# Kernel optimization log

Hardware: AMD Instinct MI355X
Metric: run time of the kernel (lower is better)

Reference implementation:

```python
import jax, jax.numpy as jnp
import numpy as np

H = 16  # num_heads

def setup_inputs() -> dict:
    key = jax.random.key(0)
    ks = jax.random.split(key, 5)
    B, L, D = 2, 2048, 1024
    x = jax.random.normal(ks[0], (B, L, D), dtype=jnp.float32)
    # causal mask: masked_fill where mask == 0
    attn_mask = jnp.tril(jnp.ones((L, L), dtype=jnp.int32))
    scale = 1.0 / np.sqrt(D)
    Wq = jax.random.normal(ks[1], (D, D), dtype=jnp.float32) * scale
    Wk = jax.random.normal(ks[2], (D, D), dtype=jnp.float32) * scale
    Wv = jax.random.normal(ks[3], (D, D), dtype=jnp.float32) * scale
    Wo = jax.random.normal(ks[4], (D, D), dtype=jnp.float32) * scale
    return {"x": x, "attn_mask": attn_mask, "Wq": Wq, "Wk": Wk, "Wv": Wv, "Wo": Wo}

def reference(x, attn_mask, Wq, Wk, Wv, Wo):
    B, L, D = x.shape
    dh = D // H
    # nn.Linear with no bias: y = x @ W^T
    q = (x @ Wq.T).reshape(B, L, H, dh)
    k = (x @ Wk.T).reshape(B, L, H, dh)
    v = (x @ Wv.T).reshape(B, L, H, dh)
    # scores: [B, H, L, L]
    scores = jnp.einsum('blhd,bmhd->bhlm', q, k) / jnp.sqrt(jnp.array(dh, x.dtype))
    scores = jnp.where(attn_mask == 0, -jnp.inf, scores)
    attn = jax.nn.softmax(scores, axis=-1)
    out = jnp.einsum('bhlm,bmhd->blhd', attn, v).reshape(B, L, D)
    return out @ Wo.T
```

## Files before the change

### kernel.cpp

```cpp
#include <hip/hip_runtime.h>
#include <math.h>

#define L_SEQ  2048
#define D_MODEL 1024
#define N_HEAD 16
#define D_HEAD 64
#define B_SIZE 2

typedef __attribute__((ext_vector_type(8))) short bf16x8;
typedef __attribute__((ext_vector_type(4))) float f32x4;
typedef unsigned short u16;
typedef unsigned int u32;

__device__ __forceinline__ f32x4 mfma16(bf16x8 a, bf16x8 b, f32x4 c) {
    return __builtin_amdgcn_mfma_f32_16x16x32_bf16(a, b, c, 0, 0, 0);
}

__device__ __forceinline__ u16 f2bf(float x) {
    u32 u = __builtin_bit_cast(u32, x);
    u32 r = (u + 0x7FFFu + ((u >> 16) & 1u)) >> 16;
    return (u16)r;
}
__device__ __forceinline__ u16 f2bf_t(float x) {
    return (u16)(__builtin_bit_cast(u32, x) >> 16);
}
__device__ __forceinline__ float bf2f(u16 h) {
    u32 u = ((u32)h) << 16;
    return __builtin_bit_cast(float, u);
}

__device__ __forceinline__ void gl2lds16(const void* g, void* l) {
    __builtin_amdgcn_global_load_lds(
        (__attribute__((address_space(1))) void*)(g),
        (__attribute__((address_space(3))) void*)(l), 16, 0, 0);
}

__global__ __launch_bounds__(256) void split_all(
    const float* __restrict__ x,
    const float* __restrict__ w0, const float* __restrict__ w1,
    const float* __restrict__ w2, const float* __restrict__ w3,
    u16* __restrict__ x2, u16* __restrict__ wout) {
    const int id = blockIdx.x;
    const float* in;
    u16* out;
    int idx;
    if (id < 4096) {
        in = x; out = x2; idx = id * 256 + threadIdx.x;
    } else {
        const int wi = (id - 4096) >> 10;
        const int blk = (id - 4096) & 1023;
        in = (wi == 0) ? w0 : (wi == 1) ? w1 : (wi == 2) ? w2 : w3;
        out = wout + (size_t)wi * 2097152;
        idx = blk * 256 + threadIdx.x;
    }
    const int c4 = idx << 2;
    const int r = c4 >> 10, c = c4 & 1023;
    float4 v = *(const float4*)(in + c4);
    u16 h0 = f2bf(v.x), h1 = f2bf(v.y), h2 = f2bf(v.z), h3 = f2bf(v.w);
    ushort4 hi = make_ushort4(h0, h1, h2, h3);
    ushort4 lo = make_ushort4(f2bf(v.x - bf2f(h0)), f2bf(v.y - bf2f(h1)),
                              f2bf(v.z - bf2f(h2)), f2bf(v.w - bf2f(h3)));
    *(ushort4*)(out + (size_t)r * 2048 + c) = hi;
    *(ushort4*)(out + (size_t)r * 2048 + 1024 + c) = lo;
}

__device__ __forceinline__ int kaOf(int x) {
    return (((x >> 4) == 1) ? 1024 : 0) + ((x << 6) & 1023);
}
__device__ __forceinline__ int kwOf(int x) {
    return (((x >> 4) == 0) ? 1024 : 0) + ((x << 6) & 1023);
}

#define SBAR()  do { __builtin_amdgcn_sched_barrier(0); \
                     __builtin_amdgcn_s_barrier(); \
                     __builtin_amdgcn_sched_barrier(0); } while (0)

__global__ __launch_bounds__(512) void gemm256_qkv(
    const u16* __restrict__ A2, const u16* __restrict__ Wall,
    u16* __restrict__ Qh, u16* __restrict__ Ql,
    u16* __restrict__ Kh, u16* __restrict__ Kl,
    u16* __restrict__ Vh) {
    extern __shared__ __align__(16) u16 smem[];

    const int t = threadIdx.x, l = t & 63, wid = t >> 6;
    const int id = blockIdx.x;
    const int wg = (id & 7) * 24 + (id >> 3);
    const int mt = wg / 12, ntile = wg % 12;
    const int m0 = mt << 8, n0 = ntile << 8;

    const int wrH = wid >> 2;
    const int wc = (wid & 3) << 6;
    const int bHalf = (wid & 3) >> 1;
    const int brB = (wid & 1) << 6;

    f32x4 acc[8][4];
#pragma unroll
    for (int i = 0; i < 8; ++i)
#pragma unroll
        for (int j = 0; j < 4; ++j) acc[i][j] = (f32x4){0.f, 0.f, 0.f, 0.f};

    const int sr = t >> 3, sc = t & 7;

    auto stageA = [&](int x, int half) {
        const int koff = kaOf(x);
        u16* dst = smem + ((x & 1) * 32768) + half * 8192;
        const u16* srcb = A2 + (size_t)(m0 + half * 128) * 2048 + koff;
#pragma unroll
        for (int p = 0; p < 2; ++p) {
            const int r = sr + p * 64;
            const int ck = sc ^ (r & 7);
            gl2lds16(srcb + (size_t)r * 2048 + ck * 8, dst + (t + p * 512) * 8);
        }
    };
    auto stageB = [&](int x, int half) {
        const int koff = kwOf(x);
        u16* dst = smem + 16384 + ((x & 1) * 32768) + half * 8192;
        const u16* srcb = Wall + (size_t)(n0 + half * 128) * 2048 + koff;
#pragma unroll
        for (int p = 0; p < 2; ++p) {
            const int r = sr + p * 64;
            const int ck = sc ^ (r & 7);
            gl2lds16(srcb + (size_t)r * 2048 + ck * 8, dst + (t + p * 512) * 8);
        }
    };
    auto dsA = [&](int s, int mh, int kc, bf16x8 af[4]) {
        const u16* Ab = smem + s * 32768 + wrH * 8192;
#pragma unroll
        for (int f = 0; f < 4; ++f) {
            const int r = mh * 64 + f * 16 + (l & 15);
            const int c8 = kc * 4 + (l >> 4);
            af[f] = *(const bf16x8*)&Ab[r * 64 + ((c8 ^ (r & 7)) << 3)];
        }
    };
    auto dsB = [&](int s, int kc, bf16x8 bfr[4]) {
        const u16* Bb = smem + 16384 + s * 32768 + bHalf * 8192;
#pragma unroll
        for (int f = 0; f < 4; ++f) {
            const int r = brB + f * 16 + (l & 15);
            const int c8 = kc * 4 + (l >> 4);
            bfr[f] = *(const bf16x8*)&Bb[r * 64 + ((c8 ^ (r & 7)) << 3)];
        }
    };

    stageB(0, 0); stageB(0, 1); stageA(0, 0); stageA(0, 1);
    stageB(1, 0); stageB(1, 1);
    __builtin_amdgcn_sched_barrier(0);
    asm volatile("s_waitcnt vmcnt(4)" ::: "memory");
    __builtin_amdgcn_s_barrier();
    __builtin_amdgcn_sched_barrier(0);

    const int NT = 48;
    bf16x8 breg0[4], breg1[4], af[4];
    for (int tt = 0; tt < NT; ++tt) {
        const int s = tt & 1;
        dsA(s, 0, 0, af); dsB(s, 0, breg0);
        if (tt + 1 < NT) stageA(tt + 1, 0);
        SBAR();
        __builtin_amdgcn_s_setprio(1);
#pragma unroll
        for (int f = 0; f < 4; ++f)
#pragma unroll
            for (int fn = 0; fn < 4; ++fn)
                acc[f][fn] = mfma16(af[f], breg0[fn], acc[f][fn]);
        __builtin_amdgcn_s_setprio(0);
        SBAR();
        dsA(s, 0, 1, af); dsB(s, 1, breg1);
        if (tt + 1 < NT) stageA(tt + 1, 1);
        SBAR();
        __builtin_amdgcn_s_setprio(1);
#pragma unroll
        for (int f = 0; f < 4; ++f)
#pragma unroll
            for (int fn = 0; fn < 4; ++fn)
                acc[f][fn] = mfma16(af[f], breg1[fn], acc[f][fn]);
        __builtin_amdgcn_s_setprio(0);
        SBAR();
        dsA(s, 1, 0, af);
        if (tt + 2 < NT) stageB(tt + 2, 0);
        SBAR();
        __builtin_amdgcn_s_setprio(1);
#pragma unroll
        for (int f = 0; f < 4; ++f)
#pragma unroll
            for (int fn = 0; fn < 4; ++fn)
                acc[4 + f][fn] = mfma16(af[f], breg0[fn], acc[4 + f][fn]);
        __builtin_amdgcn_s_setprio(0);
        SBAR();
        dsA(s, 1, 1, af);
        if (tt + 2 < NT) stageB(tt + 2, 1);
        SBAR();
        __builtin_amdgcn_s_setprio(1);
#pragma unroll
        for (int f = 0; f < 4; ++f)
#pragma unroll
            for (int fn = 0; fn < 4; ++fn)
                acc[4 + f][fn] = mfma16(af[f], breg1[fn], acc[4 + f][fn]);
        __builtin_amdgcn_s_setprio(0);
        __builtin_amdgcn_sched_barrier(0);
        if (tt + 2 < NT) {
            asm volatile("s_waitcnt vmcnt(4)" ::: "memory");
        } else if (tt + 1 < NT) {
            asm volatile("s_waitcnt vmcnt(0)" ::: "memory");
        }
        __builtin_amdgcn_s_barrier();
        __builtin_amdgcn_sched_barrier(0);
    }

#pragma unroll
    for (int fm = 0; fm < 8; ++fm)
#pragma unroll
        for (int fn = 0; fn < 4; ++fn)
#pragma unroll
            for (int rg = 0; rg < 4; ++rg) {
                const int gm = m0 + wrH * 128 + fm * 16 + ((l >> 4) << 2) + rg;
                const int gn = n0 + wc + fn * 16 + (l & 15);
                const int z = gn >> 10, col = gn & 1023;
                float v = acc[fm][fn][rg];
                if (z == 0) v *= 0.125f;
                const int b = gm >> 11, lq = gm & 2047;
                const int h = col >> 6, d = col & 63;
                const size_t oi = (((size_t)(b * 16 + h)) * 2048 + lq) * 64 + d;
                const u16 hi = f2bf(v);
                if (z == 0) { Qh[oi] = hi; Ql[oi] = f2bf(v - bf2f(hi)); }
                else if (z == 1) { Kh[oi] = hi; Kl[oi] = f2bf(v - bf2f(hi)); }
                else { Vh[oi] = hi; }
            }
}

__global__ __launch_bounds__(256) void gemm_wo(
    const u16* __restrict__ A2, const u16* __restrict__ W2,
    float* __restrict__ Cout) {
    __shared__ __align__(16) u16 As[128 * 32];
    __shared__ __align__(16) u16 Ws2[64 * 32];
    const int t = threadIdx.x, l = t & 63, wid = t >> 6;
    const int id = blockIdx.x;
    const int nid = ((id & 7) << 6) + (id >> 3);
    const int m0 = (nid >> 4) << 7;
    const int n0 = (nid & 15) << 6;
    const int wm = wid >> 1, wn = wid & 1;

    f32x4 acc[4][2];
#pragma unroll
    for (int i = 0; i < 4; ++i)
#pragma unroll
        for (int j = 0; j < 2; ++j) acc[i][j] = (f32x4){0.f, 0.f, 0.f, 0.f};

    const int arow0 = t >> 2, ach0 = (t & 3) ^ (arow0 & 3);
    const int arow1 = (t + 256) >> 2, ach1 = (t & 3) ^ (arow1 & 3);
    const int brow = t >> 2, bch = (t & 3) ^ (brow & 3);

    for (int k0 = 0; k0 < 3072; k0 += 32) {
        const int rg3 = k0 >> 10, kb = k0 & 1023;
        const int ka = (rg3 == 1 ? 1024 : 0) + kb;
        const int kw = (rg3 == 0 ? 1024 : 0) + kb;
        __syncthreads();
        gl2lds16(A2 + (size_t)(m0 + arow0) * 2048 + ka + ach0 * 8,
                 (u16*)As + t * 8);
        gl2lds16(A2 + (size_t)(m0 + arow1) * 2048 + ka + ach1 * 8,
                 (u16*)As + (t + 256) * 8);
        if (t < 256)
            gl2lds16(W2 + (size_t)(n0 + brow) * 2048 + kw + bch * 8,
                     (u16*)Ws2 + t * 8);
        __syncthreads();
        bf16x8 af[4], bfr[2];
#pragma unroll
        for (int f = 0; f < 4; ++f) {
            const int row = wm * 64 + f * 16 + (l & 15);
            const int ch = (l >> 4) ^ (row & 3);
            af[f] = *(const bf16x8*)&As[(row << 5) + (ch << 3)];
        }
#pragma unroll
        for (int f = 0; f < 2; ++f) {
            const int rown = wn * 32 + f * 16 + (l & 15);
            const int chn = (l >> 4) ^ (rown & 3);
            bfr[f] = *(const bf16x8*)&Ws2[(rown << 5) + (chn << 3)];
        }
        __builtin_amdgcn_s_setprio(1);
#pragma unroll
        for (int fm = 0; fm < 4; ++fm)
#pragma unroll
            for (int fn = 0; fn < 2; ++fn)
                acc[fm][fn] = mfma16(af[fm], bfr[fn], acc[fm][fn]);
        __builtin_amdgcn_s_setprio(0);
    }

#pragma unroll
    for (int fm = 0; fm < 4; ++fm)
#pragma unroll
        for (int fn = 0; fn < 2; ++fn)
#pragma unroll
            for (int rg = 0; rg < 4; ++rg) {
                const int gm = m0 + wm * 64 + fm * 16 + ((l >> 4) << 2) + rg;
                const int gn = n0 + wn * 32 + fn * 16 + (l & 15);
                Cout[(size_t)gm * 1024 + gn] = acc[fm][fn][rg];
            }
}

__global__ __launch_bounds__(128) void vtrans(const u16* __restrict__ Vh,
                                              u16* __restrict__ Vth) {
    const int t = threadIdx.x;
    const int kt = (blockIdx.x << 1) + (t >> 6);
    const int h = blockIdx.y, b = blockIdx.z;
    const size_t base = ((size_t)(b * 16 + h)) * 131072;
    const int kv0 = kt << 6;
    const int st = t & 63;
    const int r0 = (st >> 3) << 3;
    const int c0 = (st & 7) << 3;
    ushort4 inv[8][2];
#pragma unroll
    for (int j = 0; j < 8; ++j) {
        const u16* p = Vh + base + (size_t)(kv0 + r0 + j) * 64 + c0;
        inv[j][0] = *(const ushort4*)p;
        inv[j][1] = *(const ushort4*)(p + 4);
    }
#pragma unroll
    for (int i = 0; i < 8; ++i) {
        u16 o[8];
#pragma unroll
        for (int j = 0; j < 8; ++j) {
            ushort4 vv = inv[j][i >> 2];
            const int ii = i & 3;
            o[j] = (ii == 0) ? vv.x : (ii == 1) ? vv.y : (ii == 2) ? vv.z : vv.w;
        }
        u16* q = Vth + base + (size_t)(c0 + i) * 2048 + kv0 + r0;
        *(ushort4*)q = make_ushort4(o[0], o[1], o[2], o[3]);
        *(ushort4*)(q + 4) = make_ushort4(o[4], o[5], o[6], o[7]);
    }
}

struct QTileState {
    bf16x8 qhf[2], qlf[2];
    f32x4 oacc[4];
    float mrow[4], lrow[4];
};

__device__ __forceinline__ void qstate_init(
    QTileState& st, const u16* Qh, const u16* Ql, size_t hb, int q0, int w, int l) {
    const int rowq = q0 + (w << 4) + (l & 15);
#pragma unroll
    for (int kc = 0; kc < 2; ++kc) {
        const size_t off = hb + (size_t)rowq * 64 + (((kc << 2) + (l >> 4)) << 3);
        st.qhf[kc] = *(const bf16x8*)(Qh + off);
        st.qlf[kc] = *(const bf16x8*)(Ql + off);
    }
#pragma unroll
    for (int i = 0; i < 4; ++i) {
        st.oacc[i] = (f32x4){0.f, 0.f, 0.f, 0.f};
        st.mrow[i] = -INFINITY;
        st.lrow[i] = 0.f;
    }
}

__device__ __forceinline__ void fa_qk_softmax(
    QTileState& st, const u16* bKh, const u16* bKl,
    int kv0, int q0, int w, int l, u16 pb[4][4]) {
    f32x4 sacc[4];
#pragma unroll
    for (int nf = 0; nf < 4; ++nf) sacc[nf] = (f32x4){0.f, 0.f, 0.f, 0.f};
#pragma unroll
    for (int kc = 0; kc < 2; ++kc) {
        bf16x8 kh_[4], kl_[4];
#pragma unroll
        for (int nf = 0; nf < 4; ++nf) {
            const int row = (nf << 4) + (l & 15);
            const int ch = ((kc << 2) + (l >> 4)) ^ (row & 7);
            kh_[nf] = *(const bf16x8*)&bKh[(row << 6) + (ch << 3)];
            kl_[nf] = *(const bf16x8*)&bKl[(row << 6) + (ch << 3)];
        }
        __builtin_amdgcn_s_setprio(1);
#pragma unroll
        for (int nf = 0; nf < 4; ++nf) {
            sacc[nf] = mfma16(st.qhf[kc], kl_[nf], sacc[nf]);
            sacc[nf] = mfma16(st.qlf[kc], kh_[nf], sacc[nf]);
            sacc[nf] = mfma16(st.qhf[kc], kh_[nf], sacc[nf]);
        }
        __builtin_amdgcn_s_setprio(0);
    }

    const bool domask = (kv0 + 63) > (q0 + (w << 4));
    float pm[4] = {-INFINITY, -INFINITY, -INFINITY, -INFINITY};
    float sv[4][4];
#pragma unroll
    for (int nf = 0; nf < 4; ++nf)
#pragma unroll
        for (int rg = 0; rg < 4; ++rg) {
            float x = sacc[nf][rg];
            if (domask) {
                const int colg = kv0 + (nf << 4) + (l & 15);
                const int rowg = q0 + (w << 4) + ((l >> 4) << 2) + rg;
                if (colg > rowg) x = -INFINITY;
            }
            sv[nf][rg] = x;
            pm[rg] = fmaxf(pm[rg], x);
        }
#pragma unroll
    for (int rg = 0; rg < 4; ++rg) {
        float v = pm[rg];
        v = fmaxf(v, __shfl_xor(v, 1));
        v = fmaxf(v, __shfl_xor(v, 2));
        v = fmaxf(v, __shfl_xor(v, 4));
        v = fmaxf(v, __shfl_xor(v, 8));
        pm[rg] = v;
    }
    const float need = fmaxf(fmaxf(pm[0] - st.mrow[0], pm[1] - st.mrow[1]),
                             fmaxf(pm[2] - st.mrow[2], pm[3] - st.mrow[3]));
    if (__any(need > 8.0f)) {
#pragma unroll
        for (int rg = 0; rg < 4; ++rg) {
            const float mn = fmaxf(st.mrow[rg], pm[rg]);
            const float al = __expf(st.mrow[rg] - mn);
            st.mrow[rg] = mn;
            st.lrow[rg] *= al;
#pragma unroll
            for (int nf = 0; nf < 4; ++nf) st.oacc[nf][rg] *= al;
        }
    }
    float ps[4] = {0.f, 0.f, 0.f, 0.f};
#pragma unroll
    for (int nf = 0; nf < 4; ++nf)
#pragma unroll
        for (int rg = 0; rg < 4; ++rg) {
            const float p = __expf(sv[nf][rg] - st.mrow[rg]);
            ps[rg] += p;
            pb[nf][rg] = f2bf_t(p);
        }
#pragma unroll
    for (int rg = 0; rg < 4; ++rg) {
        float v = ps[rg];
        v += __shfl_xor(v, 1);
        v += __shfl_xor(v, 2);
        v += __shfl_xor(v, 4);
        v += __shfl_xor(v, 8);
        st.lrow[rg] += v;
    }
}

__device__ __forceinline__ void fa_writeP(const u16 pb[4][4], int l, u16* Pw) {
#pragma unroll
    for (int nf = 0; nf < 4; ++nf)
#pragma unroll
        for (int rg = 0; rg < 4; ++rg) {
            const int r = ((l >> 4) << 2) + rg;
            const int c = (nf << 4) + (l & 15);
            const int ch = (c >> 3) ^ (r & 7);
            Pw[(r << 6) + (ch << 3) + (c & 7)] = pb[nf][rg];
        }
}

__device__ __forceinline__ void fa_epilogue(
    QTileState& st, u16* A2, int g, int q0, int w, int l) {
    const int b = g >> 4, h = g & 15;
    float inv[4];
#pragma unroll
    for (int rg = 0; rg < 4; ++rg) inv[rg] = 1.0f / st.lrow[rg];
#pragma unroll
    for (int nf = 0; nf < 4; ++nf)
#pragma unroll
        for (int rg = 0; rg < 4; ++rg) {
            const int rowq = q0 + (w << 4) + ((l >> 4) << 2) + rg;
            const int m = (b << 11) + rowq;
            const int d = (nf << 4) + (l & 15);
            const float v = st.oacc[nf][rg] * inv[rg];
            const u16 hi = f2bf(v);
            const u16 lo = f2bf(v - bf2f(hi));
            const size_t rb = (size_t)m * 2048;
            A2[rb + h * 64 + d] = hi;
            A2[rb + 1024 + h * 64 + d] = lo;
        }
}

__global__ __launch_bounds__(512) void flash_mfma(
    const u16* __restrict__ Qh, const u16* __restrict__ Ql,
    const u16* __restrict__ Kh, const u16* __restrict__ Kl,
    const u16* __restrict__ Vth,
    u16* __restrict__ A2) {
    extern __shared__ __align__(16) u16 smem[];
    u16* const KhsA = smem;
    u16* const KlsA = smem + 4096;
    u16* const VhsA = smem + 8192;
    u16* const KhsB = smem + 12288;
    u16* const KlsB = smem + 16384;
    u16* const VhsB = smem + 20480;
    u16* const PsB  = smem + 24576;
    u16* const PsA  = smem + 32768;

    const int t = threadIdx.x, l = t & 63, w = t >> 6;
    const int id = blockIdx.x;
    const int nid = ((id & 7) << 5) + (id >> 3);
    const int g = nid >> 3;
    const int p = nid & 7;
    const int q0A = p << 7;
    const int q0B = (15 - p) << 7;
    const size_t hb = (size_t)g * 131072;

    QTileState stA, stB;
    qstate_init(stA, Qh, Ql, hb, q0A, w, l);
    qstate_init(stB, Qh, Ql, hb, q0B, w, l);

    const int row_s = t >> 3;
    const int cs_s = (t & 7) ^ (row_s & 7);

    auto stage = [&](u16* dKh, u16* dKl, u16* dVh, int kt_) {
        const int kv0s = kt_ << 6;
        const size_t koff = hb + (size_t)(kv0s + row_s) * 64 + cs_s * 8;
        gl2lds16(Kh + koff, dKh + t * 8);
        gl2lds16(Kl + koff, dKl + t * 8);
        const size_t voff = hb + (size_t)row_s * 2048 + kv0s + cs_s * 8;
        gl2lds16(Vth + voff, dVh + t * 8);
    };

    u16* const PwB = PsB + (w << 10);
    u16* const PwA = PsA + (w << 10);
    const int ntA = (p << 1) + 2;
    const int ntB = 32 - (p << 1);

    auto unit = [&](const u16* bKh, const u16* bKl, const u16* bVh, int kt_) {
        const int kv0 = kt_ << 6;
        const bool aB = kv0 <= q0B + (w << 4) + 15;
        const bool aA = (kt_ < ntA) && (kv0 <= q0A + (w << 4) + 15);
        if (!aB && !aA) return;
        u16 pbB[4][4], pbA[4][4];
        if (aB) fa_qk_softmax(stB, bKh, bKl, kv0, q0B, w, l, pbB);
        if (aA) fa_qk_softmax(stA, bKh, bKl, kv0, q0A, w, l, pbA);
        if (aB) fa_writeP(pbB, l, PwB);
        if (aA) fa_writeP(pbA, l, PwA);
#pragma unroll
        for (int kc = 0; kc < 2; ++kc) {
            bf16x8 vh_[4];
#pragma unroll
            for (int nf = 0; nf < 4; ++nf) {
                const int row = (nf << 4) + (l & 15);
                const int cv = ((kc << 2) + (l >> 4)) ^ (row & 7);
                vh_[nf] = *(const bf16x8*)&bVh[(row << 6) + (cv << 3)];
            }
            const int r = l & 15;
            const int chp = ((kc << 2) + (l >> 4)) ^ (r & 7);
            __builtin_amdgcn_s_setprio(1);
            if (aB) {
                const bf16x8 pa = *(const bf16x8*)&PwB[(r << 6) + (chp << 3)];
#pragma unroll
                for (int nf = 0; nf < 4; ++nf)
                    stB.oacc[nf] = mfma16(pa, vh_[nf], stB.oacc[nf]);
            }
            if (aA) {
                const bf16x8 pa = *(const bf16x8*)&PwA[(r << 6) + (chp << 3)];
#pragma unroll
                for (int nf = 0; nf < 4; ++nf)
                    stA.oacc[nf] = mfma16(pa, vh_[nf], stA.oacc[nf]);
            }
            __builtin_amdgcn_s_setprio(0);
        }
    };

    stage(KhsA, KlsA, VhsA, 0);
    __syncthreads();
    for (int kt = 0; kt < ntB; kt += 2) {
        stage(KhsB, KlsB, VhsB, kt + 1);
        unit(KhsA, KlsA, VhsA, kt);
        __syncthreads();
        if (kt + 2 < ntB) stage(KhsA, KlsA, VhsA, kt + 2);
        unit(KhsB, KlsB, VhsB, kt + 1);
        __syncthreads();
    }

    fa_epilogue(stA, A2, g, q0A, w, l);
    fa_epilogue(stB, A2, g, q0B, w, l);
}

__global__ __launch_bounds__(256) void gemm_bt_f32(
    const float* __restrict__ A, const float* __restrict__ W,
    float* __restrict__ C, int M, int N, int K) {
    __shared__ float As[16][68];
    __shared__ float Bs[16][68];
    const int t = threadIdx.x;
    const int tx = t & 15, ty = t >> 4;
    const int m0 = blockIdx.y << 6, n0 = blockIdx.x << 6;
    const int lr = t >> 2, lc = (t & 3) << 2;
    const float* Ag = A + (size_t)(m0 + lr) * K + lc;
    const float* Wg = W + (size_t)(n0 + lr) * K + lc;
    float acc[4][4];
#pragma unroll
    for (int i = 0; i < 4; ++i)
#pragma unroll
        for (int j = 0; j < 4; ++j) acc[i][j] = 0.f;
    for (int k0 = 0; k0 < K; k0 += 16) {
        const float4 av = *(const float4*)(Ag + k0);
        const float4 wv = *(const float4*)(Wg + k0);
        __syncthreads();
        As[lc + 0][lr] = av.x; As[lc + 1][lr] = av.y;
        As[lc + 2][lr] = av.z; As[lc + 3][lr] = av.w;
        Bs[lc + 0][lr] = wv.x; Bs[lc + 1][lr] = wv.y;
        Bs[lc + 2][lr] = wv.z; Bs[lc + 3][lr] = wv.w;
        __syncthreads();
#pragma unroll
        for (int kk = 0; kk < 16; ++kk) {
            const float4 a = *(const float4*)&As[kk][ty << 2];
            const float4 b = *(const float4*)&Bs[kk][tx << 2];
            acc[0][0] += a.x * b.x; acc[0][1] += a.x * b.y; acc[0][2] += a.x * b.z; acc[0][3] += a.x * b.w;
            acc[1][0] += a.y * b.x; acc[1][1] += a.y * b.y; acc[1][2] += a.y * b.z; acc[1][3] += a.y * b.w;
            acc[2][0] += a.z * b.x; acc[2][1] += a.z * b.y; acc[2][2] += a.z * b.z; acc[2][3] += a.z * b.w;
            acc[3][0] += a.w * b.x; acc[3][1] += a.w * b.y; acc[3][2] += a.w * b.z; acc[3][3] += a.w * b.w;
        }
    }
#pragma unroll
    for (int i = 0; i < 4; ++i) {
        float4 o;
        o.x = acc[i][0]; o.y = acc[i][1]; o.z = acc[i][2]; o.w = acc[i][3];
        *(float4*)&C[(size_t)(m0 + (ty << 2) + i) * N + n0 + (tx << 2)] = o;
    }
}

#define SW(row, seg) ((((seg) ^ (((row) + ((row) >> 4)) & 15)) << 2))

__global__ __launch_bounds__(256) void flash_f32(
    const float* __restrict__ Q, const float* __restrict__ K,
    const float* __restrict__ V, float* __restrict__ O) {
    __shared__ float Qs[64 * 64];
    __shared__ float KPs[64 * 64];
    __shared__ float Vs[64 * 64];
    const int t = threadIdx.x;
    const int tx = t & 15, ty = t >> 4;
    const int qt = blockIdx.x, h = blockIdx.y, b = blockIdx.z;
    const int q0 = qt << 6;
    const size_t hbase = (size_t)b * L_SEQ * D_MODEL + (size_t)h * D_HEAD;
#pragma unroll
    for (int i = 0; i < 4; ++i) {
        const int idx = t + (i << 8);
        const int rr = idx >> 4, seg = idx & 15;
        const float4 qv = *(const float4*)&Q[hbase + (size_t)(q0 + rr) * D_MODEL + (seg << 2)];
        *(float4*)&Qs[rr * 64 + SW(rr, seg)] = qv;
    }
    float m[4], lr_[4], oacc[4][4];
#pragma unroll
    for (int i = 0; i < 4; ++i) {
        m[i] = -INFINITY; lr_[i] = 0.f;
#pragma unroll
        for (int j = 0; j < 4; ++j) oacc[i][j] = 0.f;
    }
    const int ntile = qt + 1;
    for (int kt = 0; kt < ntile; ++kt) {
        const int kv0 = kt << 6;
        __syncthreads();
#pragma unroll
        for (int i = 0; i < 4; ++i) {
            const int idx = t + (i << 8);
            const int rr = idx >> 4, seg = idx & 15;
            const float4 kv = *(const float4*)&K[hbase + (size_t)(kv0 + rr) * D_MODEL + (seg << 2)];
            const float4 vv = *(const float4*)&V[hbase + (size_t)(kv0 + rr) * D_MODEL + (seg << 2)];
            *(float4*)&KPs[rr * 64 + SW(rr, seg)] = kv;
            *(float4*)&Vs[rr * 64 + SW(rr, seg)] = vv;
        }
        __syncthreads();
        float s[4][4];
#pragma unroll
        for (int i = 0; i < 4; ++i)
#pragma unroll
            for (int j = 0; j < 4; ++j) s[i][j] = 0.f;
#pragma unroll
        for (int seg = 0; seg < 16; ++seg) {
            float4 qv[4], kv[4];
#pragma unroll
            for (int i = 0; i < 4; ++i) {
                const int R = (ty << 2) + i;
                qv[i] = *(const float4*)&Qs[R * 64 + SW(R, seg)];
            }
#pragma unroll
            for (int j = 0; j < 4; ++j) {
                const int Cc = (tx << 2) + j;
                kv[j] = *(const float4*)&KPs[Cc * 64 + SW(Cc, seg)];
            }
#pragma unroll
            for (int i = 0; i < 4; ++i)
#pragma unroll
                for (int j = 0; j < 4; ++j)
                    s[i][j] += qv[i].x * kv[j].x + qv[i].y * kv[j].y +
                               qv[i].z * kv[j].z + qv[i].w * kv[j].w;
        }
        const bool diag = (kt == qt);
        float tm[4];
#pragma unroll
        for (int i = 0; i < 4; ++i) {
            tm[i] = -INFINITY;
#pragma unroll
            for (int j = 0; j < 4; ++j) {
                float sval = s[i][j] * 0.125f;
                if (diag) {
                    const int Cg = kv0 + (tx << 2) + j;
                    const int Rg = q0 + (ty << 2) + i;
                    if (Cg > Rg) sval = -INFINITY;
                }
                s[i][j] = sval;
                tm[i] = fmaxf(tm[i], sval);
            }
            tm[i] = fmaxf(tm[i], __shfl_xor(tm[i], 1));
            tm[i] = fmaxf(tm[i], __shfl_xor(tm[i], 2));
            tm[i] = fmaxf(tm[i], __shfl_xor(tm[i], 4));
            tm[i] = fmaxf(tm[i], __shfl_xor(tm[i], 8));
        }
        float p[4][4];
#pragma unroll
        for (int i = 0; i < 4; ++i) {
            const float mn = fmaxf(m[i], tm[i]);
            const float alpha = __expf(m[i] - mn);
            m[i] = mn;
            float psum = 0.f;
#pragma unroll
            for (int j = 0; j < 4; ++j) {
                p[i][j] = __expf(s[i][j] - mn);
                psum += p[i][j];
            }
            psum += __shfl_xor(psum, 1);
            psum += __shfl_xor(psum, 2);
            psum += __shfl_xor(psum, 4);
            psum += __shfl_xor(psum, 8);
            lr_[i] = lr_[i] * alpha + psum;
#pragma unroll
            for (int j = 0; j < 4; ++j) oacc[i][j] *= alpha;
        }
        __syncthreads();
#pragma unroll
        for (int i = 0; i < 4; ++i) {
            const int R = (ty << 2) + i;
            float4 pv;
            pv.x = p[i][0]; pv.y = p[i][1]; pv.z = p[i][2]; pv.w = p[i][3];
            *(float4*)&KPs[R * 64 + SW(R, tx)] = pv;
        }
        __syncthreads();
#pragma unroll
        for (int cs = 0; cs < 16; ++cs) {
            float pc[4][4];
            float4 vr[4];
#pragma unroll
            for (int i = 0; i < 4; ++i) {
                const int R = (ty << 2) + i;
                const float4 pr = *(const float4*)&KPs[R * 64 + SW(R, cs)];
                pc[i][0] = pr.x; pc[i][1] = pr.y; pc[i][2] = pr.z; pc[i][3] = pr.w;
            }
#pragma unroll
            for (int cc = 0; cc < 4; ++cc) {
                const int Cr = (cs << 2) + cc;
                vr[cc] = *(const float4*)&Vs[Cr * 64 + SW(Cr, tx)];
            }
#pragma unroll
            for (int i = 0; i < 4; ++i)
#pragma unroll
                for (int cc = 0; cc < 4; ++cc) {
                    oacc[i][0] += pc[i][cc] * vr[cc].x;
                    oacc[i][1] += pc[i][cc] * vr[cc].y;
                    oacc[i][2] += pc[i][cc] * vr[cc].z;
                    oacc[i][3] += pc[i][cc] * vr[cc].w;
                }
        }
    }
#pragma unroll
    for (int i = 0; i < 4; ++i) {
        const int R = (ty << 2) + i;
        const float invl = 1.0f / lr_[i];
        float4 o;
        o.x = oacc[i][0] * invl; o.y = oacc[i][1] * invl;
        o.z = oacc[i][2] * invl; o.w = oacc[i][3] * invl;
        *(float4*)&O[hbase + (size_t)(q0 + R) * D_MODEL + (tx << 2)] = o;
    }
}

extern "C" void kernel_launch(void* const* d_in, const int* in_sizes, int n_in,
                              void* d_out, int out_size, void* d_ws, size_t ws_size,
                              hipStream_t stream) {
    const float* x  = (const float*)d_in[0];
    const float* Wq = (const float*)d_in[2];
    const float* Wk = (const float*)d_in[3];
    const float* Wv = (const float*)d_in[4];
    const float* Wo = (const float*)d_in[5];
    float* out = (float*)d_out;

    if (ws_size >= 83886080ull) {
        char* ws = (char*)d_ws;
        u16* x2  = (u16*)(ws);
        u16* Wq2 = (u16*)(ws + 16777216);
        u16* Wo2 = (u16*)(ws + 29360128);
        u16* Qh  = (u16*)(ws + 33554432);
        u16* Ql  = (u16*)(ws + 41943040);
        u16* Kh  = (u16*)(ws + 50331648);
        u16* Kl  = (u16*)(ws + 58720256);
        u16* Vth = (u16*)(ws + 67108864);
        u16* Vh  = (u16*)d_out;

        hipFuncSetAttribute((const void*)flash_mfma,
                            hipFuncAttributeMaxDynamicSharedMemorySize, 81920);
        hipFuncSetAttribute((const void*)gemm256_qkv,
                            hipFuncAttributeMaxDynamicSharedMemorySize, 131072);

        split_all<<<8192, 256, 0, stream>>>(x, Wq, Wk, Wv, Wo, x2, Wq2);
        gemm256_qkv<<<192, 512, 131072, stream>>>(x2, Wq2, Qh, Ql, Kh, Kl, Vh);
        vtrans<<<dim3(16, 16, 2), 128, 0, stream>>>(Vh, Vth);
        flash_mfma<<<256, 512, 81920, stream>>>(Qh, Ql, Kh, Kl, Vth, x2);
        gemm_wo<<<512, 256, 0, stream>>>(x2, Wo2, out);
    } else {
        const int M = B_SIZE * L_SEQ, N = D_MODEL, Kd = D_MODEL;
        float* Qw = (float*)d_ws;
        float* Kw = Qw + (size_t)M * D_MODEL;
        float* Vw = Kw + (size_t)M * D_MODEL;
        float* Aw = Vw + (size_t)M * D_MODEL;
        dim3 gg(N / 64, M / 64);
        gemm_bt_f32<<<gg, 256, 0, stream>>>(x, Wq, Qw, M, N, Kd);
        gemm_bt_f32<<<gg, 256, 0, stream>>>(x, Wk, Kw, M, N, Kd);
        gemm_bt_f32<<<gg, 256, 0, stream>>>(x, Wv, Vw, M, N, Kd);
        flash_f32<<<dim3(L_SEQ / 64, N_HEAD, B_SIZE), 256, 0, stream>>>(Qw, Kw, Vw, Aw);
        gemm_bt_f32<<<gg, 256, 0, stream>>>(Aw, Wo, out, M, N, Kd);
    }
}
```

Before: 244.8 us.

## Retile QKV GEMM to 256x192 tiles for a 256-block grid

Changes the QKV projection GEMM tile from 256x256 to 256x192 so the grid becomes 256 blocks instead of 192, matching the CU count and avoiding a partial wave. B staging is reorganized into three 64-row thirds per k-step with adjusted LDS offsets, wait counts and fragment indexing. Per-block arithmetic intensity drops somewhat and tiles now straddle the Q/K/V boundaries, which the epilogue handles per element.

```diff
diff --git a/kernel.cpp b/kernel.cpp
--- a/kernel.cpp
+++ b/kernel.cpp
@@ -84,47 +84,42 @@
 
     const int t = threadIdx.x, l = t & 63, wid = t >> 6;
     const int id = blockIdx.x;
-    const int wg = (id & 7) * 24 + (id >> 3);
-    const int mt = wg / 12, ntile = wg % 12;
-    const int m0 = mt << 8, n0 = ntile << 8;
+    const int wg = (id & 7) * 32 + (id >> 3);
+    const int mt = wg >> 4, ntile = wg & 15;
+    const int m0 = mt << 8, n0 = ntile * 192;
 
     const int wrH = wid >> 2;
-    const int wc = (wid & 3) << 6;
-    const int bHalf = (wid & 3) >> 1;
-    const int brB = (wid & 1) << 6;
-
-    f32x4 acc[8][4];
+    const int wcN = (wid & 3) * 48;
+
+    f32x4 acc[8][3];
 #pragma unroll
     for (int i = 0; i < 8; ++i)
 #pragma unroll
-        for (int j = 0; j < 4; ++j) acc[i][j] = (f32x4){0.f, 0.f, 0.f, 0.f};
+        for (int j = 0; j < 3; ++j) acc[i][j] = (f32x4){0.f, 0.f, 0.f, 0.f};
 
     const int sr = t >> 3, sc = t & 7;
 
     auto stageA = [&](int x, int half) {
         const int koff = kaOf(x);
-        u16* dst = smem + ((x & 1) * 32768) + half * 8192;
+        u16* dst = smem + (x & 1) * 16384 + half * 8192;
         const u16* srcb = A2 + (size_t)(m0 + half * 128) * 2048 + koff;
 #pragma unroll
         for (int p = 0; p < 2; ++p) {
             const int r = sr + p * 64;
             const int ck = sc ^ (r & 7);
-            gl2lds16(srcb + (size_t)r * 2048 + ck * 8, dst + (t + p * 512) * 8);
+            gl2lds16(srcb + (size_t)r * 2048 + ck * 8, dst + t * 8 + p * 4096);
         }
     };
-    auto stageB = [&](int x, int half) {
+    auto stageB = [&](int x, int third) {
         const int koff = kwOf(x);
-        u16* dst = smem + 16384 + ((x & 1) * 32768) + half * 8192;
-        const u16* srcb = Wall + (size_t)(n0 + half * 128) * 2048 + koff;
-#pragma unroll
-        for (int p = 0; p < 2; ++p) {
-            const int r = sr + p * 64;
-            const int ck = sc ^ (r & 7);
-            gl2lds16(srcb + (size_t)r * 2048 + ck * 8, dst + (t + p * 512) * 8);
-        }
+        u16* dst = smem + 32768 + (x & 1) * 12288 + third * 4096;
+        const int r = sr;
+        const int ck = sc ^ (r & 7);
+        const u16* src = Wall + (size_t)(n0 + third * 64 + r) * 2048 + koff + ck * 8;
+        gl2lds16(src, dst + t * 8);
     };
     auto dsA = [&](int s, int mh, int kc, bf16x8 af[4]) {
-        const u16* Ab = smem + s * 32768 + wrH * 8192;
+        const u16* Ab = smem + s * 16384 + wrH * 8192;
 #pragma unroll
         for (int f = 0; f < 4; ++f) {
             const int r = mh * 64 + f * 16 + (l & 15);
@@ -132,25 +127,27 @@
             af[f] = *(const bf16x8*)&Ab[r * 64 + ((c8 ^ (r & 7)) << 3)];
         }
     };
-    auto dsB = [&](int s, int kc, bf16x8 bfr[4]) {
-        const u16* Bb = smem + 16384 + s * 32768 + bHalf * 8192;
-#pragma unroll
-        for (int f = 0; f < 4; ++f) {
-            const int r = brB + f * 16 + (l & 15);
+    auto dsB = [&](int s, int kc, bf16x8 bfr[3]) {
+        const u16* Bb = smem + 32768 + s * 12288;
+#pragma unroll
+        for (int f = 0; f < 3; ++f) {
+            const int row = wcN + f * 16 + (l & 15);
+            const int third = row >> 6, lr = row & 63;
             const int c8 = kc * 4 + (l >> 4);
-            bfr[f] = *(const bf16x8*)&Bb[r * 64 + ((c8 ^ (r & 7)) << 3)];
+            bfr[f] = *(const bf16x8*)&Bb[third * 4096 + lr * 64 + ((c8 ^ (lr & 7)) << 3)];
         }
     };
 
-    stageB(0, 0); stageB(0, 1); stageA(0, 0); stageA(0, 1);
-    stageB(1, 0); stageB(1, 1);
+    stageB(0, 0); stageB(0, 1); stageB(0, 2);
+    stageA(0, 0); stageA(0, 1);
+    stageB(1, 0); stageB(1, 1); stageB(1, 2);
     __builtin_amdgcn_sched_barrier(0);
-    asm volatile("s_waitcnt vmcnt(4)" ::: "memory");
+    asm volatile("s_waitcnt vmcnt(3)" ::: "memory");
     __builtin_amdgcn_s_barrier();
     __builtin_amdgcn_sched_barrier(0);
 
     const int NT = 48;
-    bf16x8 breg0[4], breg1[4], af[4];
+    bf16x8 breg0[3], breg1[3], af[4];
     for (int tt = 0; tt < NT; ++tt) {
         const int s = tt & 1;
         dsA(s, 0, 0, af); dsB(s, 0, breg0);
@@ -160,7 +157,7 @@
 #pragma unroll
         for (int f = 0; f < 4; ++f)
 #pragma unroll
-            for (int fn = 0; fn < 4; ++fn)
+            for (int fn = 0; fn < 3; ++fn)
                 acc[f][fn] = mfma16(af[f], breg0[fn], acc[f][fn]);
         __builtin_amdgcn_s_setprio(0);
         SBAR();
@@ -171,34 +168,34 @@
 #pragma unroll
         for (int f = 0; f < 4; ++f)
 #pragma unroll
-            for (int fn = 0; fn < 4; ++fn)
+            for (int fn = 0; fn < 3; ++fn)
                 acc[f][fn] = mfma16(af[f], breg1[fn], acc[f][fn]);
         __builtin_amdgcn_s_setprio(0);
         SBAR();
         dsA(s, 1, 0, af);
-        if (tt + 2 < NT) stageB(tt + 2, 0);
+        if (tt + 2 < NT) { stageB(tt + 2, 0); stageB(tt + 2, 1); }
         SBAR();
         __builtin_amdgcn_s_setprio(1);
 #pragma unroll
         for (int f = 0; f < 4; ++f)
 #pragma unroll
-            for (int fn = 0; fn < 4; ++fn)
+            for (int fn = 0; fn < 3; ++fn)
                 acc[4 + f][fn] = mfma16(af[f], breg0[fn], acc[4 + f][fn]);
         __builtin_amdgcn_s_setprio(0);
         SBAR();
         dsA(s, 1, 1, af);
-        if (tt + 2 < NT) stageB(tt + 2, 1);
+        if (tt + 2 < NT) stageB(tt + 2, 2);
         SBAR();
         __builtin_amdgcn_s_setprio(1);
 #pragma unroll
         for (int f = 0; f < 4; ++f)
 #pragma unroll
-            for (int fn = 0; fn < 4; ++fn)
+            for (int fn = 0; fn < 3; ++fn)
                 acc[4 + f][fn] = mfma16(af[f], breg1[fn], acc[4 + f][fn]);
         __builtin_amdgcn_s_setprio(0);
         __builtin_amdgcn_sched_barrier(0);
         if (tt + 2 < NT) {
-            asm volatile("s_waitcnt vmcnt(4)" ::: "memory");
+            asm volatile("s_waitcnt vmcnt(3)" ::: "memory");
         } else if (tt + 1 < NT) {
             asm volatile("s_waitcnt vmcnt(0)" ::: "memory");
         }
@@ -209,11 +206,11 @@
 #pragma unroll
     for (int fm = 0; fm < 8; ++fm)
 #pragma unroll
-        for (int fn = 0; fn < 4; ++fn)
+        for (int fn = 0; fn < 3; ++fn)
 #pragma unroll
             for (int rg = 0; rg < 4; ++rg) {
                 const int gm = m0 + wrH * 128 + fm * 16 + ((l >> 4) << 2) + rg;
-                const int gn = n0 + wc + fn * 16 + (l & 15);
+                const int gn = n0 + wcN + fn * 16 + (l & 15);
                 const int z = gn >> 10, col = gn & 1023;
                 float v = acc[fm][fn][rg];
                 if (z == 0) v *= 0.125f;
@@ -788,10 +785,10 @@
         hipFuncSetAttribute((const void*)flash_mfma,
                             hipFuncAttributeMaxDynamicSharedMemorySize, 81920);
         hipFuncSetAttribute((const void*)gemm256_qkv,
-                            hipFuncAttributeMaxDynamicSharedMemorySize, 131072);
+                            hipFuncAttributeMaxDynamicSharedMemorySize, 114688);
 
         split_all<<<8192, 256, 0, stream>>>(x, Wq, Wk, Wv, Wo, x2, Wq2);
-        gemm256_qkv<<<192, 512, 131072, stream>>>(x2, Wq2, Qh, Ql, Kh, Kl, Vh);
+        gemm256_qkv<<<256, 512, 114688, stream>>>(x2, Wq2, Qh, Ql, Kh, Kl, Vh);
         vtrans<<<dim3(16, 16, 2), 128, 0, stream>>>(Vh, Vth);
         flash_mfma<<<256, 512, 81920, stream>>>(Qh, Ql, Kh, Kl, Vth, x2);
         gemm_wo<<<512, 256, 0, stream>>>(x2, Wo2, out);
```

Measured after the change: 231.8 us. -5.3%, faster.
